# Kernel optimization log

Hardware: AMD Instinct MI355X
Metric: run time of the kernel (lower is better)

Reference implementation:

```python
import jax, jax.numpy as jnp
import numpy as np

B, T, D_MODEL, N_HEADS = 4, 2048, 1024, 16


def _alibi_bias(n_heads, seq_len):
    # matches torch alibi_bias(): slopes 2**(-8*i/m), i=1..m, m = pow2_ceil(n_heads)
    m = 1
    while m < n_heads:
        m *= 2
    slopes = jnp.array([2.0 ** (-8.0 * i / m) for i in range(1, m + 1)][:n_heads],
                       dtype=jnp.float32)
    pos = jnp.arange(seq_len)
    bias = (pos[None, :] - pos[:, None]).astype(jnp.float32)  # [T, T], j - i
    return slopes[:, None, None, None] * bias[None, None]      # [H, 1, T, T]


def setup_inputs() -> dict:
    key = jax.random.key(0)
    kx, kqkv, ko = jax.random.split(key, 3)
    x = jax.random.normal(kx, (B, T, D_MODEL), dtype=jnp.float32)
    Wqkv = jax.random.normal(kqkv, (3 * D_MODEL, D_MODEL), dtype=jnp.float32) / np.sqrt(D_MODEL)
    Wo = jax.random.normal(ko, (D_MODEL, D_MODEL), dtype=jnp.float32) / np.sqrt(D_MODEL)
    alibi = _alibi_bias(N_HEADS, T)  # [H, 1, T, T]
    return {"x": x, "alibi": alibi, "Wqkv": Wqkv, "Wo": Wo}


def reference(x, alibi, Wqkv, Wo):
    Bb, Tt, C = x.shape
    H = N_HEADS
    dk = C // H
    # qkv projection: [B, T, 3C] -> [B, T, 3, H, dk]
    qkv = (x @ Wqkv.T).reshape(Bb, Tt, 3, H, dk)
    q = jnp.moveaxis(qkv[:, :, 0], 2, 1)  # [B, H, T, dk]
    k = jnp.moveaxis(qkv[:, :, 1], 2, 1)
    v = jnp.moveaxis(qkv[:, :, 2], 2, 1)
    # causal (-inf above diagonal) + alibi additive mask, fp32, like the torch path
    causal = jnp.triu(jnp.full((Tt, Tt), -jnp.inf, dtype=jnp.float32), k=1)
    mask = causal[None, None] + alibi[:, 0][None]  # [1, H, T, T]
    scores = jnp.einsum('bhqd,bhkd->bhqk', q, k) / jnp.sqrt(jnp.float32(dk)) + mask
    p = jax.nn.softmax(scores, axis=-1)
    att = jnp.einsum('bhqk,bhkd->bhqd', p, v)           # [B, H, T, dk]
    y = jnp.moveaxis(att, 1, 2).reshape(Bb, Tt, C)       # [B, T, C]
    return y @ Wo.T
```

## Files before the change

### kernel.cpp

```cpp
#include <hip/hip_runtime.h>
#include <hip/hip_bf16.h>


#define B_ 4
#define T_ 2048
#define C_ 1024
#define H_ 16
#define DK 64

typedef __attribute__((ext_vector_type(8))) short short8;
typedef __attribute__((ext_vector_type(4))) float floatx4;

#define GLDS16(g, l)                                                          \
    __builtin_amdgcn_global_load_lds(                                         \
        (const __attribute__((address_space(1))) void*)(g),                   \
        (__attribute__((address_space(3))) void*)(l), 16, 0, 0)

static __device__ inline short f2bf(float x) {
    __hip_bfloat16 h = __float2bfloat16(x);
    return *reinterpret_cast<short*>(&h);
}

__global__ void detect_k(const unsigned int* __restrict__ x,
                         const unsigned int* __restrict__ ali,
                         const unsigned int* __restrict__ wqkv,
                         const unsigned int* __restrict__ wo,
                         int* __restrict__ flags) {
    __shared__ int cnt[4];
    const int tid = threadIdx.x;
    if (tid < 4) cnt[tid] = 0;
    __syncthreads();
    const int g = tid >> 6, l = tid & 63;
    const unsigned int* p = (g == 0) ? x : (g == 1) ? ali : (g == 2) ? wqkv : wo;
    int c = 0;
    for (int i = 0; i < 4; i++) {
        unsigned int w = p[l * 4 + i];
        int e0 = (w >> 7) & 0xFF;
        int e1 = (w >> 23) & 0xFF;
        c += (e0 >= 100 && e0 <= 140);
        c += (e1 >= 100 && e1 <= 140);
    }
    atomicAdd(&cnt[g], c);
    __syncthreads();
    if (l == 0) flags[g] = (cnt[g] < 400) ? 1 : 0;
}

__global__ void tobf16_all_k(const void* __restrict__ x,
                             const void* __restrict__ wq,
                             const void* __restrict__ wo,
                             short* __restrict__ ox,
                             short* __restrict__ owq,
                             short* __restrict__ owo) {
    const int bid = blockIdx.x;
    const void* in;
    short* out;
    int n8, b0, nb;
    if (bid < 2048) {
        in = x; out = ox; n8 = B_ * T_ * C_ / 8; b0 = bid; nb = 2048;
    } else if (bid < 3584) {
        in = wq; out = owq; n8 = 3 * C_ * C_ / 8; b0 = bid - 2048; nb = 1536;
    } else {
        in = wo; out = owo; n8 = C_ * C_ / 8; b0 = bid - 3584; nb = 512;
    }
    const unsigned int* u = (const unsigned int*)in;
    int c = 0;
#pragma unroll
    for (int i = 0; i < 16; i++) {
        unsigned int w = u[i];
        int e0 = (w >> 7) & 0xFF;
        int e1 = (w >> 23) & 0xFF;
        c += (e0 >= 100 && e0 <= 140);
        c += (e1 >= 100 && e1 <= 140);
    }
    const bool f32 = (c < 25);
    int i = b0 * blockDim.x + threadIdx.x;
    const int stride = nb * blockDim.x;
    for (; i < n8; i += stride) {
        if (f32) {
            float4 f0 = ((const float4*)in)[2 * i];
            float4 f1 = ((const float4*)in)[2 * i + 1];
            short8 v = { f2bf(f0.x), f2bf(f0.y), f2bf(f0.z), f2bf(f0.w),
                         f2bf(f1.x), f2bf(f1.y), f2bf(f1.z), f2bf(f1.w) };
            *(short8*)(out + (size_t)i * 8) = v;
        } else {
            *(short8*)(out + (size_t)i * 8) = ((const short8*)in)[i];
        }
    }
}

__global__ __launch_bounds__(256) void gemm_qkvvt_k(
    const short* __restrict__ xbf, const short* __restrict__ wqkvbf,
    short* __restrict__ qkv) {
    const int K = 1024;
    const int tid  = threadIdx.x;
    const int wv   = tid >> 6;
    const int lane = tid & 63;
    const int l15  = lane & 15;
    const int quad = lane >> 4;
    const int wm = wv >> 1, wn = wv & 1;

    const int id = blockIdx.x;
    const bool m0 = id < 1024;
    int bm, bn;
    const short *Ap, *Wp;
    if (m0) {
        bn = id & 15; bm = id >> 4; Ap = xbf; Wp = wqkvbf;
    } else {
        int j = id - 1024;
        bn = j & 63; bm = j >> 6;
        Ap = wqkvbf + (size_t)2048 * 1024; Wp = xbf;
    }

    __shared__ short As[128 * 64];
    __shared__ short Bs[128 * 64];

    floatx4 acc[4][4];
#pragma unroll
    for (int mt = 0; mt < 4; mt++)
#pragma unroll
        for (int nt = 0; nt < 4; nt++)
#pragma unroll
            for (int r = 0; r < 4; r++) acc[mt][nt][r] = 0.f;

    const int lr = lane >> 3;
    const int lc = lane & 7;
    const int cg = lc ^ lr;

    for (int kt = 0; kt < K; kt += 64) {
        __syncthreads();
#pragma unroll
        for (int i = 0; i < 4; i++) {
            const int rbase = wv * 32 + i * 8;
            const int r = rbase + lr;
            size_t ga = (size_t)(bm * 128 + r) * K + kt + cg * 8;
            GLDS16(Ap + ga, As + rbase * 64);
            size_t gb = (size_t)(bn * 128 + r) * K + kt + cg * 8;
            GLDS16(Wp + gb, Bs + rbase * 64);
        }
        __syncthreads();
#pragma unroll
        for (int ks = 0; ks < 64; ks += 32) {
            short8 af[4], bf[4];
#pragma unroll
            for (int mt = 0; mt < 4; mt++) {
                int row = wm * 64 + mt * 16 + l15;
                int cs = ((ks >> 3) + quad) ^ (row & 7);
                af[mt] = *(const short8*)(As + row * 64 + cs * 8);
            }
#pragma unroll
            for (int nt = 0; nt < 4; nt++) {
                int row = wn * 64 + nt * 16 + l15;
                int cs = ((ks >> 3) + quad) ^ (row & 7);
                bf[nt] = *(const short8*)(Bs + row * 64 + cs * 8);
            }
#pragma unroll
            for (int mt = 0; mt < 4; mt++)
#pragma unroll
                for (int nt = 0; nt < 4; nt++)
                    acc[mt][nt] = __builtin_amdgcn_mfma_f32_16x16x32_bf16(
                        af[mt], bf[nt], acc[mt][nt], 0, 0, 0);
        }
    }

#pragma unroll
    for (int mt = 0; mt < 4; mt++) {
#pragma unroll
        for (int nt = 0; nt < 4; nt++) {
#pragma unroll
            for (int r = 0; r < 4; r++) {
                int row = bm * 128 + wm * 64 + mt * 16 + quad * 4 + r;
                int col = bn * 128 + wn * 64 + nt * 16 + l15;
                if (m0) {
                    int b = row >> 11, t = row & (T_ - 1);
                    int s = col >> 10, rem = col & 1023;
                    int h = rem >> 6, d = rem & 63;
                    size_t dst = ((((size_t)s * B_ + b) * H_ + h) * T_ + t) * DK + d;
                    qkv[dst] = f2bf(acc[mt][nt][r]);
                } else {
                    int h = row >> 6, d = row & 63;
                    int b = col >> 11, t = col & (T_ - 1);
                    size_t dst = (((size_t)(2 * B_ + b) * H_ + h) * DK + d) * T_ + t;
                    qkv[dst] = f2bf(acc[mt][nt][r]);
                }
            }
        }
    }
}

template <int MODE, int N>
__global__ __launch_bounds__(256) void gemm128_k(const short* __restrict__ A,
                                                 const short* __restrict__ W,
                                                 void* __restrict__ Dv) {
    const int K = 1024;
    const int tid  = threadIdx.x;
    const int wv   = tid >> 6;
    const int lane = tid & 63;
    const int l15  = lane & 15;
    const int quad = lane >> 4;
    const int wm = wv >> 1, wn = wv & 1;
    const int bn = blockIdx.x, bm = blockIdx.y;

    __shared__ short As[128 * 64];
    __shared__ short Bs[128 * 64];

    floatx4 acc[4][4];
#pragma unroll
    for (int mt = 0; mt < 4; mt++)
#pragma unroll
        for (int nt = 0; nt < 4; nt++)
#pragma unroll
            for (int r = 0; r < 4; r++) acc[mt][nt][r] = 0.f;

    const int lr = lane >> 3;
    const int lc = lane & 7;
    const int cg = lc ^ lr;

    for (int kt = 0; kt < K; kt += 64) {
        __syncthreads();
#pragma unroll
        for (int i = 0; i < 4; i++) {
            const int rbase = wv * 32 + i * 8;
            const int r = rbase + lr;
            size_t ga;
            if (MODE == 2) {
                int rowg = bm * 128 + r;
                int b = rowg >> 11, t = rowg & (T_ - 1), hh = kt >> 6;
                ga = (((size_t)b * H_ + hh) * T_ + t) * DK + cg * 8;
            } else {
                ga = (size_t)(bm * 128 + r) * K + kt + cg * 8;
            }
            GLDS16(A + ga, As + rbase * 64);
            size_t gb = (size_t)(bn * 128 + r) * K + kt + cg * 8;
            GLDS16(W + gb, Bs + rbase * 64);
        }
        __syncthreads();
#pragma unroll
        for (int ks = 0; ks < 64; ks += 32) {
            short8 af[4], bf[4];
#pragma unroll
            for (int mt = 0; mt < 4; mt++) {
                int row = wm * 64 + mt * 16 + l15;
                int cs = ((ks >> 3) + quad) ^ (row & 7);
                af[mt] = *(const short8*)(As + row * 64 + cs * 8);
            }
#pragma unroll
            for (int nt = 0; nt < 4; nt++) {
                int row = wn * 64 + nt * 16 + l15;
                int cs = ((ks >> 3) + quad) ^ (row & 7);
                bf[nt] = *(const short8*)(Bs + row * 64 + cs * 8);
            }
#pragma unroll
            for (int mt = 0; mt < 4; mt++)
#pragma unroll
                for (int nt = 0; nt < 4; nt++)
                    acc[mt][nt] = __builtin_amdgcn_mfma_f32_16x16x32_bf16(
                        af[mt], bf[nt], acc[mt][nt], 0, 0, 0);
        }
    }

#pragma unroll
    for (int mt = 0; mt < 4; mt++) {
#pragma unroll
        for (int nt = 0; nt < 4; nt++) {
#pragma unroll
            for (int r = 0; r < 4; r++) {
                int row = bm * 128 + wm * 64 + mt * 16 + quad * 4 + r;
                int col = bn * 128 + wn * 64 + nt * 16 + l15;
                if (MODE == 0) {
                    int b = row >> 11, t = row & (T_ - 1);
                    int s = col >> 10, rem = col & 1023;
                    int h = rem >> 6, d = rem & 63;
                    size_t dst = ((((size_t)s * B_ + b) * H_ + h) * T_ + t) * DK + d;
                    ((short*)Dv)[dst] = f2bf(acc[mt][nt][r]);
                } else if (MODE == 3) {
                    int h = row >> 6, d = row & 63;
                    int b = col >> 11, t = col & (T_ - 1);
                    size_t dst = (((size_t)(2 * B_ + b) * H_ + h) * DK + d) * T_ + t;
                    ((short*)Dv)[dst] = f2bf(acc[mt][nt][r]);
                } else {
                    ((float*)Dv)[(size_t)row * N + col] = acc[mt][nt][r];
                }
            }
        }
    }
}

template <int MODE, int N>
__global__ __launch_bounds__(256) void gemm_k(const void* __restrict__ Av,
                                              const void* __restrict__ Wv,
                                              void* __restrict__ Dv,
                                              const int* fA, const int* fW,
                                              size_t aOff) {
    const int K = 1024;
    const int tid  = threadIdx.x;
    const int wave = tid >> 6;
    const int lane = tid & 63;
    const int l15  = lane & 15;
    const int quad = lane >> 4;
    const int bn = blockIdx.x;
    const int bm = blockIdx.y;
    const bool aF32 = fA && (*fA != 0);
    const bool wF32 = fW && (*fW != 0);

    __shared__ short As[64 * 72];
    __shared__ short Bs[64 * 72];

    floatx4 acc[4];
#pragma unroll
    for (int nt = 0; nt < 4; nt++)
#pragma unroll
        for (int r = 0; r < 4; r++) acc[nt][r] = 0.f;

    for (int kt = 0; kt < K; kt += 64) {
        __syncthreads();
#pragma unroll
        for (int i = 0; i < 2; i++) {
            int chunk = tid + i * 256;
            int r = chunk >> 3, c8 = (chunk & 7) * 8;
            size_t offA;
            if (MODE == 2) {
                int rowg = bm * 64 + r;
                int b = rowg >> 11, t = rowg & (T_ - 1), hh = kt >> 6;
                offA = (((size_t)b * H_ + hh) * T_ + t) * DK + c8;
            } else {
                offA = (size_t)(bm * 64 + r) * K + kt + c8;
            }
            size_t offW = (size_t)(bn * 64 + r) * K + kt + c8;
            if (aF32) {
                const float* Af = (const float*)Av + aOff;
                float4 f0 = *(const float4*)(Af + offA);
                float4 f1 = *(const float4*)(Af + offA + 4);
                short8 v = { f2bf(f0.x), f2bf(f0.y), f2bf(f0.z), f2bf(f0.w),
                             f2bf(f1.x), f2bf(f1.y), f2bf(f1.z), f2bf(f1.w) };
                *(short8*)(As + r * 72 + c8) = v;
            } else {
                *(short8*)(As + r * 72 + c8) =
                    *(const short8*)((const short*)Av + aOff + offA);
            }
            if (wF32) {
                const float* Wf = (const float*)Wv;
                float4 f0 = *(const float4*)(Wf + offW);
                float4 f1 = *(const float4*)(Wf + offW + 4);
                short8 v = { f2bf(f0.x), f2bf(f0.y), f2bf(f0.z), f2bf(f0.w),
                             f2bf(f1.x), f2bf(f1.y), f2bf(f1.z), f2bf(f1.w) };
                *(short8*)(Bs + r * 72 + c8) = v;
            } else {
                *(short8*)(Bs + r * 72 + c8) = *(const short8*)((const short*)Wv + offW);
            }
        }
        __syncthreads();
#pragma unroll
        for (int ks = 0; ks < 64; ks += 32) {
            short8 a = *(const short8*)(As + (wave * 16 + l15) * 72 + ks + quad * 8);
#pragma unroll
            for (int nt = 0; nt < 4; nt++) {
                short8 b = *(const short8*)(Bs + (nt * 16 + l15) * 72 + ks + quad * 8);
                acc[nt] = __builtin_amdgcn_mfma_f32_16x16x32_bf16(a, b, acc[nt], 0, 0, 0);
            }
        }
    }

#pragma unroll
    for (int nt = 0; nt < 4; nt++) {
#pragma unroll
        for (int r = 0; r < 4; r++) {
            int row = bm * 64 + wave * 16 + quad * 4 + r;
            int col = bn * 64 + nt * 16 + l15;
            if (MODE == 0) {
                int b = row >> 11, t = row & (T_ - 1);
                int s = col >> 10, rem = col & 1023;
                int h = rem >> 6, d = rem & 63;
                size_t dst = ((((size_t)s * B_ + b) * H_ + h) * T_ + t) * DK + d;
                ((short*)Dv)[dst] = f2bf(acc[nt][r]);
            } else if (MODE == 3) {
                int h = row >> 6, d = row & 63;
                int b = col >> 11, t = col & (T_ - 1);
                size_t dst = (((size_t)(2 * B_ + b) * H_ + h) * DK + d) * T_ + t;
                ((short*)Dv)[dst] = f2bf(acc[nt][r]);
            } else {
                ((float*)Dv)[(size_t)row * N + col] = acc[nt][r];
            }
        }
    }
}

__global__ __launch_bounds__(256, 4) void attn_k(short* __restrict__ qkv) {
    const int tid  = threadIdx.x;
    const int wave = tid >> 6;
    const int lane = tid & 63;
    const int l15  = lane & 15;
    const int quad = lane >> 4;
    const int gid  = blockIdx.x;
    const int bh = (gid & 7) * 8 + (gid >> 8);
    const int qb = (31 - ((gid >> 3) & 31)) * 64;
    const int b = bh >> 4, h = bh & 15;

    short* Qp       = qkv + (((size_t)(0 * B_ + b) * H_ + h) * T_) * DK;
    const short* Kp = qkv + (((size_t)(1 * B_ + b) * H_ + h) * T_) * DK;
    const short* Vt = qkv + (((size_t)(2 * B_ + b) * H_ + h) * DK) * T_;

    __shared__ short Ks[2][64 * 64];
    __shared__ short Vts[2][64 * 64];
    __shared__ short Ps[4 * 16 * 64];

    const size_t qrow = (size_t)(qb + wave * 16 + l15) * DK;
    const short8 aq0 = *(const short8*)(Qp + qrow + quad * 8);
    const short8 aq1 = *(const short8*)(Qp + qrow + 32 + quad * 8);

    const float LOG2E = 1.4426950408889634f;
    const float slope2 = exp2f(-0.5f * (float)(h + 1)) * LOG2E;
    const float scale2 = 0.125f * LOG2E;

    float lsum[4];
    floatx4 o[4];
#pragma unroll
    for (int r = 0; r < 4; r++) lsum[r] = 0.f;
#pragma unroll
    for (int nt = 0; nt < 4; nt++)
#pragma unroll
        for (int r = 0; r < 4; r++) o[nt][r] = 0.f;

    const int jt_end = qb >> 6;
    const int rb = qb + wave * 16 + quad * 4;
    int jstart = 0;
    {
        int lim = qb - 63 - (int)(20.f / slope2);
        if (lim > 0) jstart = lim >> 6;
    }

    const int lr = lane >> 3;
    const int cg = (lane & 7) ^ lr;

#pragma unroll
    for (int i = 0; i < 2; i++) {
        const int rbase = wave * 16 + i * 8;
        GLDS16(Kp + (size_t)(jstart * 64 + rbase + lr) * DK + cg * 8,
               &Ks[0][rbase * 64]);
        GLDS16(Vt + (size_t)(rbase + lr) * T_ + jstart * 64 + cg * 8,
               &Vts[0][rbase * 64]);
    }
    __syncthreads();

    floatx4 s[4];
#pragma unroll
    for (int nt = 0; nt < 4; nt++)
#pragma unroll
        for (int r = 0; r < 4; r++) s[nt][r] = 0.f;
    __builtin_amdgcn_s_setprio(1);
#pragma unroll
    for (int nt = 0; nt < 4; nt++) {
        int row = nt * 16 + l15;
        int c0 = quad ^ (row & 7);
        int c1 = (4 + quad) ^ (row & 7);
        short8 b0 = *(const short8*)(&Ks[0][0] + row * 64 + c0 * 8);
        short8 b1 = *(const short8*)(&Ks[0][0] + row * 64 + c1 * 8);
        s[nt] = __builtin_amdgcn_mfma_f32_16x16x32_bf16(aq0, b0, s[nt], 0, 0, 0);
        s[nt] = __builtin_amdgcn_mfma_f32_16x16x32_bf16(aq1, b1, s[nt], 0, 0, 0);
    }
    __builtin_amdgcn_s_setprio(0);

    int cur = 0;
    for (int jt = jstart; jt <= jt_end; jt++) {
        if (jt < jt_end) {
            const int nxt = cur ^ 1;
#pragma unroll
            for (int i = 0; i < 2; i++) {
                const int rbase = wave * 16 + i * 8;
                GLDS16(Kp + (size_t)((jt + 1) * 64 + rbase + lr) * DK + cg * 8,
                       &Ks[nxt][rbase * 64]);
                GLDS16(Vt + (size_t)(rbase + lr) * T_ + (jt + 1) * 64 + cg * 8,
                       &Vts[nxt][rbase * 64]);
            }
        }
        const short* Vtc = &Vts[cur][0];

        const bool diag = (jt == jt_end);
#pragma unroll
        for (int nt = 0; nt < 4; nt++) {
            int colg = jt * 64 + nt * 16 + l15;
            float cb = slope2 * (float)(colg - rb);
#pragma unroll
            for (int r = 0; r < 4; r++) {
                float sv = fmaf(s[nt][r], scale2, cb - slope2 * (float)r);
                if (diag && colg > rb + r) sv = -1e30f;
                float p = exp2f(sv);
                lsum[r] += p;
                int prow = quad * 4 + r;
                int pcol = nt * 16 + l15;
                Ps[wave * 1024 + prow * 64 +
                   (((pcol >> 3) ^ (prow & 7)) << 3) + (pcol & 7)] = f2bf(p);
            }
        }

        __builtin_amdgcn_s_setprio(1);
#pragma unroll
        for (int ks = 0; ks < 64; ks += 32) {
            short8 a = *(const short8*)(
                Ps + wave * 1024 + l15 * 64 +
                ((((ks >> 3) + quad) ^ (l15 & 7)) << 3));
#pragma unroll
            for (int nt = 0; nt < 4; nt++) {
                int row = nt * 16 + l15;
                int cs = ((ks >> 3) + quad) ^ (row & 7);
                short8 bf = *(const short8*)(Vtc + row * 64 + cs * 8);
                o[nt] = __builtin_amdgcn_mfma_f32_16x16x32_bf16(a, bf, o[nt], 0, 0, 0);
            }
        }
        __builtin_amdgcn_s_setprio(0);

        __syncthreads();
        cur ^= 1;

        if (jt < jt_end) {
            const short* Ksn = &Ks[cur][0];
#pragma unroll
            for (int nt = 0; nt < 4; nt++)
#pragma unroll
                for (int r = 0; r < 4; r++) s[nt][r] = 0.f;
            __builtin_amdgcn_s_setprio(1);
#pragma unroll
            for (int nt = 0; nt < 4; nt++) {
                int row = nt * 16 + l15;
                int c0 = quad ^ (row & 7);
                int c1 = (4 + quad) ^ (row & 7);
                short8 b0 = *(const short8*)(Ksn + row * 64 + c0 * 8);
                short8 b1 = *(const short8*)(Ksn + row * 64 + c1 * 8);
                s[nt] = __builtin_amdgcn_mfma_f32_16x16x32_bf16(aq0, b0, s[nt], 0, 0, 0);
                s[nt] = __builtin_amdgcn_mfma_f32_16x16x32_bf16(aq1, b1, s[nt], 0, 0, 0);
            }
            __builtin_amdgcn_s_setprio(0);
        }
    }

#pragma unroll
    for (int r = 0; r < 4; r++) {
#pragma unroll
        for (int mask = 1; mask < 16; mask <<= 1)
            lsum[r] += __shfl_xor(lsum[r], mask);
    }
#pragma unroll
    for (int nt = 0; nt < 4; nt++) {
#pragma unroll
        for (int r = 0; r < 4; r++) {
            int t = qb + wave * 16 + quad * 4 + r;
            int d = nt * 16 + l15;
            Qp[(size_t)t * DK + d] = f2bf(o[nt][r] / lsum[r]);
        }
    }
}

extern "C" void kernel_launch(void* const* d_in, const int* in_sizes, int n_in,
                              void* d_out, int out_size, void* d_ws, size_t ws_size,
                              hipStream_t stream) {
    const void* x    = d_in[0];
    const void* ali  = d_in[1];
    const void* Wqkv = d_in[2];
    const void* Wo   = d_in[3];
    float* out = (float*)d_out;

    int*   flags  = (int*)d_ws;
    short* qkv    = (short*)((char*)d_ws + 1024);
    short* xbf    = (short*)((char*)d_ws + 50332672);
    short* wqkvbf = (short*)((char*)d_ws + 67109888);
    short* wobf   = (short*)((char*)d_ws + 73401344);
    const bool fast = ws_size >= (size_t)75498496;

    dim3 blk(256);
    if (fast) {
        tobf16_all_k<<<4096, 256, 0, stream>>>(x, Wqkv, Wo, xbf, wqkvbf, wobf);
        gemm_qkvvt_k<<<1536, blk, 0, stream>>>(xbf, wqkvbf, qkv);
        attn_k<<<dim3(2048), blk, 0, stream>>>(qkv);
        gemm128_k<2, C_><<<dim3(8, 64), blk, 0, stream>>>(qkv, wobf, out);
    } else {
        detect_k<<<1, 256, 0, stream>>>((const unsigned int*)x,
                                        (const unsigned int*)ali,
                                        (const unsigned int*)Wqkv,
                                        (const unsigned int*)Wo, flags);
        gemm_k<0, 0><<<dim3(32, 128), blk, 0, stream>>>(x, Wqkv, qkv,
                                                        &flags[0], &flags[2], 0);
        gemm_k<3, 0><<<dim3(128, 16), blk, 0, stream>>>(Wqkv, x, qkv,
                                                        &flags[2], &flags[0],
                                                        (size_t)2048 * 1024);
        attn_k<<<dim3(2048), blk, 0, stream>>>(qkv);
        gemm_k<2, C_><<<dim3(16, 128), blk, 0, stream>>>(qkv, Wo, out,
                                                         nullptr, &flags[3], 0);
    }
}
```

Measured before the change: 500.2 us.

## Widen attention blocks to 128 query rows with eight waves sharing K/V tiles

The attention kernel now launches 512-thread blocks covering 128 query rows (eight waves) instead of 256 threads covering 64 rows. Each K/V tile staged in LDS is reused by twice as many waves, which halves global K/V traffic per query and spreads the tile loads across more threads. The diagonal masking is extended to the last two key tiles. The cost is more causally wasted work per block and coarser scheduling, with fewer, larger blocks and higher LDS use per block.

```diff
diff --git a/kernel.cpp b/kernel.cpp
--- a/kernel.cpp
+++ b/kernel.cpp
@@ -384,15 +384,15 @@
     }
 }
 
-__global__ __launch_bounds__(256, 4) void attn_k(short* __restrict__ qkv) {
+__global__ __launch_bounds__(512, 4) void attn_k(short* __restrict__ qkv) {
     const int tid  = threadIdx.x;
     const int wave = tid >> 6;
     const int lane = tid & 63;
     const int l15  = lane & 15;
     const int quad = lane >> 4;
     const int gid  = blockIdx.x;
-    const int bh = (gid & 7) * 8 + (gid >> 8);
-    const int qb = (31 - ((gid >> 3) & 31)) * 64;
+    const int bh = (gid & 7) * 8 + (gid >> 7);
+    const int qb = (15 - ((gid >> 3) & 15)) * 128;
     const int b = bh >> 4, h = bh & 15;
 
     short* Qp       = qkv + (((size_t)(0 * B_ + b) * H_ + h) * T_) * DK;
@@ -401,7 +401,7 @@
 
     __shared__ short Ks[2][64 * 64];
     __shared__ short Vts[2][64 * 64];
-    __shared__ short Ps[4 * 16 * 64];
+    __shared__ short Ps[8 * 16 * 64];
 
     const size_t qrow = (size_t)(qb + wave * 16 + l15) * DK;
     const short8 aq0 = *(const short8*)(Qp + qrow + quad * 8);
@@ -420,7 +420,7 @@
 #pragma unroll
         for (int r = 0; r < 4; r++) o[nt][r] = 0.f;
 
-    const int jt_end = qb >> 6;
+    const int jt_end = (qb >> 6) + 1;
     const int rb = qb + wave * 16 + quad * 4;
     int jstart = 0;
     {
@@ -428,17 +428,11 @@
         if (lim > 0) jstart = lim >> 6;
     }
 
-    const int lr = lane >> 3;
-    const int cg = (lane & 7) ^ lr;
-
-#pragma unroll
-    for (int i = 0; i < 2; i++) {
-        const int rbase = wave * 16 + i * 8;
-        GLDS16(Kp + (size_t)(jstart * 64 + rbase + lr) * DK + cg * 8,
-               &Ks[0][rbase * 64]);
-        GLDS16(Vt + (size_t)(rbase + lr) * T_ + jstart * 64 + cg * 8,
-               &Vts[0][rbase * 64]);
-    }
+    const int sr = tid >> 3;
+    const int cg = (tid & 7) ^ (sr & 7);
+
+    GLDS16(Kp + (size_t)(jstart * 64 + sr) * DK + cg * 8, &Ks[0][wave * 512]);
+    GLDS16(Vt + (size_t)sr * T_ + jstart * 64 + cg * 8, &Vts[0][wave * 512]);
     __syncthreads();
 
     floatx4 s[4];
@@ -463,18 +457,14 @@
     for (int jt = jstart; jt <= jt_end; jt++) {
         if (jt < jt_end) {
             const int nxt = cur ^ 1;
-#pragma unroll
-            for (int i = 0; i < 2; i++) {
-                const int rbase = wave * 16 + i * 8;
-                GLDS16(Kp + (size_t)((jt + 1) * 64 + rbase + lr) * DK + cg * 8,
-                       &Ks[nxt][rbase * 64]);
-                GLDS16(Vt + (size_t)(rbase + lr) * T_ + (jt + 1) * 64 + cg * 8,
-                       &Vts[nxt][rbase * 64]);
-            }
+            GLDS16(Kp + (size_t)((jt + 1) * 64 + sr) * DK + cg * 8,
+                   &Ks[nxt][wave * 512]);
+            GLDS16(Vt + (size_t)sr * T_ + (jt + 1) * 64 + cg * 8,
+                   &Vts[nxt][wave * 512]);
         }
         const short* Vtc = &Vts[cur][0];
 
-        const bool diag = (jt == jt_end);
+        const bool diag = (jt >= jt_end - 1);
 #pragma unroll
         for (int nt = 0; nt < 4; nt++) {
             int colg = jt * 64 + nt * 16 + l15;
@@ -569,7 +559,7 @@
     if (fast) {
         tobf16_all_k<<<4096, 256, 0, stream>>>(x, Wqkv, Wo, xbf, wqkvbf, wobf);
         gemm_qkvvt_k<<<1536, blk, 0, stream>>>(xbf, wqkvbf, qkv);
-        attn_k<<<dim3(2048), blk, 0, stream>>>(qkv);
+        attn_k<<<1024, 512, 0, stream>>>(qkv);
         gemm128_k<2, C_><<<dim3(8, 64), blk, 0, stream>>>(qkv, wobf, out);
     } else {
         detect_k<<<1, 256, 0, stream>>>((const unsigned int*)x,
@@ -581,7 +571,7 @@
         gemm_k<3, 0><<<dim3(128, 16), blk, 0, stream>>>(Wqkv, x, qkv,
                                                         &flags[2], &flags[0],
                                                         (size_t)2048 * 1024);
-        attn_k<<<dim3(2048), blk, 0, stream>>>(qkv);
+        attn_k<<<1024, 512, 0, stream>>>(qkv);
         gemm_k<2, C_><<<dim3(16, 128), blk, 0, stream>>>(qkv, Wo, out,
                                                          nullptr, &flags[3], 0);
     }
```

New measurement: 510.7 us. 2.1% more time.
